# Optimization experiments

Measured on AMD Instinct MI355X. Metric: run time of the kernel, lower is better.

Reference implementation:

```python
import jax, jax.numpy as jnp
import numpy as np


def ste_round(x):
    # straight-through rounding (identity gradient), as used in brevitas fake-quant
    return x + jax.lax.stop_gradient(jnp.round(x) - x)


def quant_weight(w, bits):
    # symmetric per-tensor int quantization: scale = max|w| / (2^(b-1)-1)
    qmax = 2.0 ** (bits - 1) - 1.0
    s = jnp.max(jnp.abs(w)) / qmax
    return jnp.clip(ste_round(w / s), -qmax, qmax) * s


def quant_relu(x, scale, bits):
    # unsigned act quant (QuantReLU): clip to [0, scale], round to 2^b-1 levels
    n = 2.0 ** bits - 1.0
    step = scale / n
    return ste_round(jnp.clip(x, 0.0, scale) / step) * step


def conv2d(x, w, b, pad):
    # NCHW 'same' conv, stride 1
    y = jax.lax.conv_general_dilated(
        x, w, window_strides=(1, 1),
        padding=[(pad, pad), (pad, pad)],
        dimension_numbers=('NCHW', 'OIHW', 'NCHW'))
    return y + b[None, :, None, None]


def setup_inputs() -> dict:
    key = jax.random.key(0)
    ks = jax.random.split(key, 8)
    B, H, W = 8, 512, 512
    x = jax.random.uniform(ks[0], (B, 1, H, W), dtype=jnp.float32)
    # xavier-ish init scales: gain / sqrt(fan_in + fan_out per kernel elem)
    w1 = jax.random.normal(ks[1], (64, 1, 9, 9), dtype=jnp.float32) * 0.12
    b1 = jax.random.normal(ks[2], (64,), dtype=jnp.float32) * 0.01
    w2 = jax.random.normal(ks[3], (32, 64, 5, 5), dtype=jnp.float32) * 0.03
    b2 = jax.random.normal(ks[4], (32,), dtype=jnp.float32) * 0.01
    w3 = jax.random.normal(ks[5], (1, 32, 5, 5), dtype=jnp.float32) * 0.05
    b3 = jax.random.normal(ks[6], (1,), dtype=jnp.float32) * 0.01
    # activation quant scales (learned params in brevitas; fixed here)
    s1 = jnp.ones((1,), dtype=jnp.float32) * 4.0
    s2 = jnp.ones((1,), dtype=jnp.float32) * 4.0
    s3 = jnp.ones((1,), dtype=jnp.float32) * 2.0
    return {"x": x, "w1": w1, "b1": b1, "w2": w2, "b2": b2,
            "w3": w3, "b3": b3, "s1": s1, "s2": s2, "s3": s3}


def reference(x, w1, b1, w2, b2, w3, b3, s1, s2, s3):
    NBK, NBA, NLACT = 8, 8, 8
    # conv1: 1->64, k=9, pad=4, int8 weights; quant-ReLU (nba bits)
    h = conv2d(x, quant_weight(w1, NBK), b1, pad=4)
    h = quant_relu(h, s1[0], NBA)
    # conv2: 64->32, k=5, pad=2
    h = conv2d(h, quant_weight(w2, NBK), b2, pad=2)
    h = quant_relu(h, s2[0], NBA)
    # conv3: 32->1, k=5, pad=2, last-layer weight bits = nlact = 8
    h = conv2d(h, quant_weight(w3, NLACT), b3, pad=2)
    h = quant_relu(h, s3[0], NLACT)
    return h
```

## Files before the change

kernel.cpp:

```cpp
#include <hip/hip_runtime.h>
#include <cmath>

#define HH 512
#define WW 512
#define BB 8
#define WP (WW + 4)
#define HP (HH + 4)

#define PROWS 520
#define PCOLS 528
#define PT ((size_t)BB * PROWS * PCOLS)

typedef int v4i __attribute__((ext_vector_type(4)));
typedef float v4f __attribute__((ext_vector_type(4)));
typedef _Float16 v8h __attribute__((ext_vector_type(8)));

#if defined(__has_builtin)
#if __has_builtin(__builtin_amdgcn_sdot4)
#define DOT4(a, b, c) __builtin_amdgcn_sdot4((a), (b), (c), false)
#endif
#endif
#ifndef DOT4
static __device__ __forceinline__ int dot4_fb(int a, int b, int c) {
  c += ((a << 24) >> 24) * ((b << 24) >> 24);
  c += ((a << 16) >> 24) * ((b << 16) >> 24);
  c += ((a << 8) >> 24) * ((b << 8) >> 24);
  c += (a >> 24) * (b >> 24);
  return c;
}
#define DOT4(a, b, c) dot4_fb((a), (b), (c))
#endif

static constexpr size_t SCALES_OFF = 0;
static constexpr size_t CORRF_OFF  = 64;
static constexpr size_t FS3_OFF    = 512;
static constexpr size_t QW1_OFF    = 1024;
static constexpr size_t W1FRAG_OFF = 24576;
static constexpr size_t W2S_OFF    = 65536;
static constexpr size_t W3P_OFF    = 131072;
static constexpr size_t H1_OFF     = (size_t)1 << 20;
static constexpr size_t H1_SZ      = (size_t)BB * HP * WP * 64;
static constexpr size_t H2_OFF     = H1_OFF + H1_SZ;
static constexpr size_t H2_SZ      = (size_t)BB * HP * WP * 32;
static constexpr size_t WS_NEED    = H2_OFF + H2_SZ;

__global__ void quant_weights_k(const float* __restrict__ w1,
                                const float* __restrict__ w2,
                                const float* __restrict__ w3,
                                float* __restrict__ scales,
                                float* __restrict__ qw1,
                                signed char* __restrict__ w2s,
                                signed char* __restrict__ w3p) {
  const int t = blockIdx.x;
  const float* src = (t == 0) ? w1 : (t == 1) ? w2 : w3;
  const int n = (t == 0) ? 64 * 81 : (t == 1) ? 32 * 64 * 25 : 32 * 25;
  __shared__ float red[256];
  float m = 0.0f;
  for (int i = threadIdx.x; i < n; i += 256) m = fmaxf(m, fabsf(src[i]));
  red[threadIdx.x] = m;
  __syncthreads();
  for (int s = 128; s > 0; s >>= 1) {
    if ((int)threadIdx.x < s) red[threadIdx.x] = fmaxf(red[threadIdx.x], red[threadIdx.x + s]);
    __syncthreads();
  }
  const float scale = red[0] / 127.0f;
  if (threadIdx.x == 0) scales[t] = scale;
  for (int i = threadIdx.x; i < n; i += 256) {
    float q = rintf(src[i] / scale);
    q = fminf(fmaxf(q, -127.0f), 127.0f);
    if (t == 0) {
      qw1[i] = q;
    } else if (t == 1) {
      const int oc = i / 1600;
      const int r = i - oc * 1600;
      const int ic = r / 25, tap = r - ic * 25;
      w2s[(((tap * 4 + (ic >> 4)) * 32) + oc) * 16 + (ic & 15)] = (signed char)(int)q;
    } else {
      const int ic = i / 25, tap = i - ic * 25;
      w3p[tap * 32 + ic] = (signed char)(int)q;
    }
  }
}

__global__ void prep_k(const signed char* __restrict__ w2s,
                       const signed char* __restrict__ w3p,
                       const float* __restrict__ qw1,
                       int* __restrict__ corrf, int* __restrict__ fs3,
                       unsigned short* __restrict__ w1frag) {
  const int tid = threadIdx.x;
  if (tid < 32) {
    int s = 0;
    for (int tap = 0; tap < 25; ++tap)
      for (int kb = 0; kb < 4; ++kb)
        for (int j = 0; j < 16; ++j)
          s += (int)w2s[((tap * 4 + kb) * 32 + tid) * 16 + j];
    corrf[tid] = s;
  } else if (tid == 32) {
    int s = 0;
    for (int i = 0; i < 800; ++i) s += (int)w3p[i];
    fs3[0] = s;
  }
  for (int i = tid; i < 18432; i += 256) {
    const int e = i & 7, lidx = (i >> 3) & 63, nn = (i >> 9) & 3, j = i >> 11;
    const int t = j * 32 + (lidx >> 4) * 8 + e;
    const int term = (t >= 144) ? 1 : 0;
    const int rem = t - term * 144;
    const int ky = rem >> 4, kx = rem & 15;
    const int oc = nn * 16 + (lidx & 15);
    float v = 0.0f;
    if (kx < 9) v = qw1[oc * 81 + ky * 9 + kx];
    if (term) v *= (1.0f / 4096.0f);
    const _Float16 hv = (_Float16)v;
    w1frag[i] = __builtin_bit_cast(unsigned short, hv);
  }
}

__global__ __launch_bounds__(256) void prep_x_k(const float* __restrict__ x,
                                                unsigned short* __restrict__ planes) {
  const size_t i = (size_t)blockIdx.x * 256 + threadIdx.x;
  if (i >= PT) return;
  const int col = (int)(i % PCOLS);
  const size_t t = i / PCOLS;
  const int row = (int)(t % PROWS);
  const int b = (int)(t / PROWS);
  const float* xb = x + (size_t)b * HH * WW;
  const int xr = row - 4;
  float v0 = 0.0f, v1 = 0.0f;
  if (xr >= 0 && xr < HH) {
    const int c0 = col - 4, c1 = col - 3;
    if (c0 >= 0 && c0 < WW) v0 = xb[(size_t)xr * WW + c0];
    if (c1 >= 0 && c1 < WW) v1 = xb[(size_t)xr * WW + c1];
  }
  const _Float16 h0 = (_Float16)v0;
  const _Float16 l0 = (_Float16)((v0 - (float)h0) * 4096.0f);
  const _Float16 h1 = (_Float16)v1;
  const _Float16 l1 = (_Float16)((v1 - (float)h1) * 4096.0f);
  planes[i]          = __builtin_bit_cast(unsigned short, h0);
  planes[PT + i]     = __builtin_bit_cast(unsigned short, l0);
  planes[2 * PT + i] = __builtin_bit_cast(unsigned short, h1);
  planes[3 * PT + i] = __builtin_bit_cast(unsigned short, l1);
}

__global__ void fill_k(unsigned char* __restrict__ h1p, unsigned char* __restrict__ h2p) {
  const int idx = blockIdx.x * 256 + threadIdx.x;
  const uint4 v = make_uint4(0x80808080u, 0x80808080u, 0x80808080u, 0x80808080u);
  if (idx < 66048) {
    const int q = idx & 3; const int u = idx >> 2;
    const int pxi = u % WP; const int rr = u / WP;
    const int bb = rr >> 2, sel = rr & 3;
    const int row = (sel < 2) ? sel : 512 + sel;
    *(uint4*)(h1p + (((size_t)bb * HP + row) * WP + pxi) * 64 + q * 16) = v;
  } else if (idx < 131584) {
    const int e = idx - 66048; const int q = e & 3; int u = e >> 2;
    const int c = u & 3; u >>= 2;
    const int row = 2 + (u & 511); const int bb = u >> 9;
    const int col = (c < 2) ? c : 512 + c;
    *(uint4*)(h1p + (((size_t)bb * HP + row) * WP + col) * 64 + q * 16) = v;
  } else if (idx < 164608) {
    const int e = idx - 131584; const int q = e & 1; const int u = e >> 1;
    const int pxi = u % WP; const int rr = u / WP;
    const int bb = rr >> 2, sel = rr & 3;
    const int row = (sel < 2) ? sel : 512 + sel;
    *(uint4*)(h2p + (((size_t)bb * HP + row) * WP + pxi) * 32 + q * 16) = v;
  } else {
    const int e = idx - 164608; const int q = e & 1; int u = e >> 1;
    const int c = u & 3; u >>= 2;
    const int row = 2 + (u & 511); const int bb = u >> 9;
    const int col = (c < 2) ? c : 512 + c;
    *(uint4*)(h2p + (((size_t)bb * HP + row) * WP + col) * 32 + q * 16) = v;
  }
}

__global__ __launch_bounds__(512) void conv1_k(
    const unsigned short* __restrict__ planes,
    const unsigned short* __restrict__ w1frag,
    const float* __restrict__ b1,
    const float* __restrict__ scales,
    const float* __restrict__ s1,
    unsigned char* __restrict__ h1p) {
  __shared__ alignas(16) unsigned short wf[18432];
  for (int i = threadIdx.x; i < 2304; i += 512)
    ((int4*)wf)[i] = ((const int4*)w1frag)[i];
  __syncthreads();

  const int y = blockIdx.x & (HH - 1);
  const int b = blockIdx.x >> 9;
  const int l = threadIdx.x & 63;
  const int wv = threadIdx.x >> 6;
  const int pxw = wv * 64;
  const int r = l & 15, kb = l >> 4;

  const unsigned short* pb = planes + (size_t)(r & 1) * (2 * PT)
                           + ((size_t)b * PROWS + y) * PCOLS + (pxw + (r & ~1));
  int offs[9];
  #pragma unroll
  for (int j = 0; j < 9; ++j) {
    const int t0 = j * 32 + kb * 8;
    const int term = (t0 >= 144) ? 1 : 0;
    const int rem = t0 - term * 144;
    offs[j] = term * (int)PT + (rem >> 4) * PCOLS + (rem & 8);
  }

  v4f acc[4][4];
  #pragma unroll
  for (int m = 0; m < 4; ++m)
    #pragma unroll
    for (int n = 0; n < 4; ++n) acc[m][n] = (v4f){0.f, 0.f, 0.f, 0.f};

  #pragma unroll
  for (int j = 0; j < 9; ++j) {
    v8h av[4];
    #pragma unroll
    for (int m = 0; m < 4; ++m) {
      const void* ap = __builtin_assume_aligned((const void*)(pb + offs[j] + m * 16), 4);
      uint4 tv;
      __builtin_memcpy(&tv, ap, 16);
      av[m] = __builtin_bit_cast(v8h, tv);
    }
    #pragma unroll
    for (int n = 0; n < 4; ++n) {
      const v8h bv = *(const v8h*)(wf + ((size_t)(j * 4 + n) * 64 + l) * 8);
      #pragma unroll
      for (int m = 0; m < 4; ++m)
        acc[m][n] = __builtin_amdgcn_mfma_f32_16x16x32_f16(av[m], bv, acc[m][n], 0, 0, 0);
    }
  }

  const float ws1 = scales[0];
  const float sc = s1[0], step = sc / 255.0f;
  unsigned char* orow = h1p + (((size_t)b * HP + y + 2) * WP + 2) * 64;
  #pragma unroll
  for (int n = 0; n < 4; ++n) {
    const int oc = n * 16 + r;
    const float bias = b1[oc];
    #pragma unroll
    for (int m = 0; m < 4; ++m) {
      #pragma unroll
      for (int reg = 0; reg < 4; ++reg) {
        const int px = pxw + m * 16 + kb * 4 + reg;
        const float h = acc[m][n][reg] * ws1 + bias;
        const float c = fminf(fmaxf(h, 0.0f), sc);
        int qi = (int)rintf(c / step);
        qi = qi < 0 ? 0 : (qi > 255 ? 255 : qi);
        orow[(size_t)px * 64 + oc] = (unsigned char)(qi ^ 0x80);
      }
    }
  }
}

__global__ __launch_bounds__(256) void conv2_k(
    const unsigned char* __restrict__ h1p,
    const int4* __restrict__ w2s,
    const int* __restrict__ corrf,
    const float* __restrict__ b2,
    const float* __restrict__ scales,
    const float* __restrict__ s1, const float* __restrict__ s2,
    unsigned char* __restrict__ h2p) {
  __shared__ alignas(16) signed char wlds[51200];
  __shared__ int clds[32];
  {
    int4* dst = (int4*)wlds;
    for (int i = threadIdx.x; i < 3200; i += 256) dst[i] = w2s[i];
    if (threadIdx.x < 32) clds[threadIdx.x] = corrf[threadIdx.x];
  }
  __syncthreads();

  const int l = threadIdx.x & 63;
  const int wv = threadIdx.x >> 6;
  const int r = l & 15, kb = l >> 4;
  const int y = blockIdx.y * 4;
  const int b = blockIdx.z;
  const int xw = blockIdx.x * 64 + wv * 16;

  v4i acc[4][2];
  #pragma unroll
  for (int t = 0; t < 4; ++t)
    #pragma unroll
    for (int n = 0; n < 2; ++n) acc[t][n] = (v4i){0, 0, 0, 0};

  const size_t rstride = (size_t)WP * 64;
  const unsigned char* abase = h1p + (((size_t)b * HP + y) * WP + xw + r) * 64 + kb * 16;

  v4i a_cur[8], a_nxt[8];
  #pragma unroll
  for (int j = 0; j < 8; ++j) a_cur[j] = *(const v4i*)(abase + j * rstride);

  #pragma unroll
  for (int kx = 0; kx < 5; ++kx) {
    if (kx < 4) {
      #pragma unroll
      for (int j = 0; j < 8; ++j)
        a_nxt[j] = *(const v4i*)(abase + (kx + 1) * 64 + j * rstride);
    }
    const signed char* bcol = wlds + kx * 2048 + kb * 512 + r * 16;
    #pragma unroll
    for (int ky = 0; ky < 5; ++ky) {
      const v4i bf0 = *(const v4i*)(bcol + ky * 10240);
      const v4i bf1 = *(const v4i*)(bcol + ky * 10240 + 256);
      #pragma unroll
      for (int t = 0; t < 4; ++t) {
        acc[t][0] = __builtin_amdgcn_mfma_i32_16x16x64_i8(a_cur[ky + t], bf0, acc[t][0], 0, 0, 0);
        acc[t][1] = __builtin_amdgcn_mfma_i32_16x16x64_i8(a_cur[ky + t], bf1, acc[t][1], 0, 0, 0);
      }
    }
    if (kx < 4) {
      #pragma unroll
      for (int j = 0; j < 8; ++j) a_cur[j] = a_nxt[j];
    }
  }

  const float step1 = s1[0] / 255.0f;
  const float sc2 = s2[0], step2 = sc2 / 255.0f;
  const float asc = step1 * scales[1];
  #pragma unroll
  for (int n = 0; n < 2; ++n) {
    const int oc = n * 16 + r;
    const float bias = b2[oc];
    const int c128 = clds[oc] * 128;
    #pragma unroll
    for (int t = 0; t < 4; ++t) {
      unsigned char* orow = h2p + (((size_t)b * HP + y + t + 2) * WP + xw + 2) * 32;
      #pragma unroll
      for (int reg = 0; reg < 4; ++reg) {
        const int pxi = kb * 4 + reg;
        const float v = (float)(acc[t][n][reg] + c128) * asc + bias;
        const float c = fminf(fmaxf(v, 0.0f), sc2);
        int qi = (int)rintf(c / step2);
        qi = qi < 0 ? 0 : (qi > 255 ? 255 : qi);
        orow[(size_t)pxi * 32 + oc] = (unsigned char)(qi ^ 0x80);
      }
    }
  }
}

__global__ __launch_bounds__(256) void conv3_k(
    const unsigned char* __restrict__ h2p,
    const signed char* __restrict__ w3p,
    const int* __restrict__ fs3,
    const float* __restrict__ b3,
    const float* __restrict__ scales,
    const float* __restrict__ s2, const float* __restrict__ s3,
    float* __restrict__ out) {
  const int p  = blockIdx.x * 256 + threadIdx.x;
  const int px = p & (WW - 1);
  const int py = (p >> 9) & (HH - 1);
  const int bz = p >> 18;

  int acc = 0;
  const unsigned char* base = h2p + (((size_t)bz * HP + py) * WP + px) * 32;
  #pragma unroll
  for (int ky = 0; ky < 5; ++ky) {
    const unsigned char* rp = base + (size_t)ky * WP * 32;
    #pragma unroll
    for (int kx = 0; kx < 5; ++kx) {
      const int* ap = (const int*)(rp + kx * 32);
      const int* wp = (const int*)(w3p + (ky * 5 + kx) * 32);
      #pragma unroll
      for (int g = 0; g < 8; ++g) acc = DOT4(ap[g], wp[g], acc);
    }
  }

  const int tot = acc + fs3[0] * 128;
  const float step2 = s2[0] / 255.0f;
  const float sc3 = s3[0], step3 = sc3 / 255.0f;
  const float y = (float)tot * (step2 * scales[2]) + b3[0];
  const float c = fminf(fmaxf(y, 0.0f), sc3);
  float q = rintf(c / step3);
  q = fminf(fmaxf(q, 0.0f), 255.0f);
  out[p] = q * step3;
}

extern "C" void kernel_launch(void* const* d_in, const int* in_sizes, int n_in,
                              void* d_out, int out_size, void* d_ws, size_t ws_size,
                              hipStream_t stream) {
  const float* x  = (const float*)d_in[0];
  const float* w1 = (const float*)d_in[1];
  const float* b1 = (const float*)d_in[2];
  const float* w2 = (const float*)d_in[3];
  const float* b2 = (const float*)d_in[4];
  const float* w3 = (const float*)d_in[5];
  const float* b3 = (const float*)d_in[6];
  const float* s1 = (const float*)d_in[7];
  const float* s2 = (const float*)d_in[8];
  const float* s3 = (const float*)d_in[9];

  if (ws_size < WS_NEED) return;

  char* ws = (char*)d_ws;
  float*          scales  = (float*)(ws + SCALES_OFF);
  int*            corrf   = (int*)(ws + CORRF_OFF);
  int*            fs3     = (int*)(ws + FS3_OFF);
  float*          qw1     = (float*)(ws + QW1_OFF);
  unsigned short* w1frag  = (unsigned short*)(ws + W1FRAG_OFF);
  signed char*    w2s     = (signed char*)(ws + W2S_OFF);
  signed char*    w3p     = (signed char*)(ws + W3P_OFF);
  unsigned char*  h1p     = (unsigned char*)(ws + H1_OFF);
  unsigned char*  h2p     = (unsigned char*)(ws + H2_OFF);
  unsigned short* planes  = (unsigned short*)(ws + H2_OFF);

  quant_weights_k<<<3, 256, 0, stream>>>(w1, w2, w3, scales, qw1, w2s, w3p);
  prep_k<<<1, 256, 0, stream>>>(w2s, w3p, qw1, corrf, fs3, w1frag);
  prep_x_k<<<(int)(PT / 256), 256, 0, stream>>>(x, planes);

  conv1_k<<<BB * HH, 512, 0, stream>>>(planes, w1frag, b1, scales, s1, h1p);
  fill_k<<<771, 256, 0, stream>>>(h1p, h2p);

  dim3 g2(8, 128, BB);
  conv2_k<<<g2, 256, 0, stream>>>(h1p, (const int4*)w2s, corrf, b2, scales, s1, s2, h2p);

  const int npix = BB * HH * WW;
  conv3_k<<<npix / 256, 256, 0, stream>>>(h2p, w3p, fs3, b3, scales, s2, s3, (float*)d_out);
}
```

Before: 429.2 us.

## Stage conv1 input tiles in LDS and vectorize conv3 activation loads

conv1 now gives each block a 2-row by 256-pixel tile. The block cooperatively loads all four shifted input planes for that tile into shared memory, and the MFMA A-fragments are then read from LDS instead of global memory, so overlapping global reads are reused across waves. The launch grid changes to match the new tiling. conv3 loads each row's 10 int4 vectors at once and then runs the dot4 products from registers. This adds LDS pressure, which may reduce occupancy in conv1.

```diff
diff --git a/kernel.cpp b/kernel.cpp
--- a/kernel.cpp
+++ b/kernel.cpp
@@ -179,26 +179,46 @@
     const float* __restrict__ s1,
     unsigned char* __restrict__ h1p) {
   __shared__ alignas(16) unsigned short wf[18432];
+  __shared__ alignas(16) unsigned int atile_dw[5440];
+
   for (int i = threadIdx.x; i < 2304; i += 512)
     ((int4*)wf)[i] = ((const int4*)w1frag)[i];
+
+  const int y0  = blockIdx.y * 2;
+  const int xt0 = blockIdx.x * 256;
+  const int b   = blockIdx.z;
+  {
+    const unsigned int* psrc = (const unsigned int*)planes;
+    #pragma unroll
+    for (int it = 0; it < 11; ++it) {
+      const int s = threadIdx.x + it * 512;
+      if (s < 5440) {
+        const int col2 = s % 136;
+        const int rp = s / 136;
+        const int row = rp % 10;
+        const int pt = rp / 10;
+        const size_t gplane = ((size_t)(pt & 1) * 2 + (size_t)(pt >> 1)) * PT;
+        const size_t gsi = gplane + ((size_t)(b * PROWS + y0 + row) * PCOLS + xt0);
+        atile_dw[s] = psrc[gsi / 2 + col2];
+      }
+    }
+  }
   __syncthreads();
 
-  const int y = blockIdx.x & (HH - 1);
-  const int b = blockIdx.x >> 9;
+  const unsigned short* atile = (const unsigned short*)atile_dw;
   const int l = threadIdx.x & 63;
-  const int wv = threadIdx.x >> 6;
-  const int pxw = wv * 64;
+  const int wave = threadIdx.x >> 6;
+  const int wrow = wave & 1, wx = wave >> 1;
   const int r = l & 15, kb = l >> 4;
 
-  const unsigned short* pb = planes + (size_t)(r & 1) * (2 * PT)
-                           + ((size_t)b * PROWS + y) * PCOLS + (pxw + (r & ~1));
+  const int base_l = (r & 1) * 2720 + wrow * 272 + (wx * 64 + (r & ~1));
   int offs[9];
   #pragma unroll
   for (int j = 0; j < 9; ++j) {
     const int t0 = j * 32 + kb * 8;
     const int term = (t0 >= 144) ? 1 : 0;
     const int rem = t0 - term * 144;
-    offs[j] = term * (int)PT + (rem >> 4) * PCOLS + (rem & 8);
+    offs[j] = term * 5440 + (rem >> 4) * 272 + (rem & 8);
   }
 
   v4f acc[4][4];
@@ -209,12 +229,12 @@
 
   #pragma unroll
   for (int j = 0; j < 9; ++j) {
+    const unsigned short* ab = atile + base_l + offs[j];
     v8h av[4];
     #pragma unroll
     for (int m = 0; m < 4; ++m) {
-      const void* ap = __builtin_assume_aligned((const void*)(pb + offs[j] + m * 16), 4);
       uint4 tv;
-      __builtin_memcpy(&tv, ap, 16);
+      __builtin_memcpy(&tv, __builtin_assume_aligned((const void*)(ab + m * 16), 4), 16);
       av[m] = __builtin_bit_cast(v8h, tv);
     }
     #pragma unroll
@@ -228,7 +248,7 @@
 
   const float ws1 = scales[0];
   const float sc = s1[0], step = sc / 255.0f;
-  unsigned char* orow = h1p + (((size_t)b * HP + y + 2) * WP + 2) * 64;
+  unsigned char* orow = h1p + (((size_t)b * HP + y0 + wrow + 2) * WP + 2 + xt0 + wx * 64) * 64;
   #pragma unroll
   for (int n = 0; n < 4; ++n) {
     const int oc = n * 16 + r;
@@ -237,7 +257,7 @@
     for (int m = 0; m < 4; ++m) {
       #pragma unroll
       for (int reg = 0; reg < 4; ++reg) {
-        const int px = pxw + m * 16 + kb * 4 + reg;
+        const int px = m * 16 + kb * 4 + reg;
         const float h = acc[m][n][reg] * ws1 + bias;
         const float c = fminf(fmaxf(h, 0.0f), sc);
         int qi = (int)rintf(c / step);
@@ -346,17 +366,24 @@
   const int py = (p >> 9) & (HH - 1);
   const int bz = p >> 18;
 
+  const int* wq = (const int*)w3p;
+  const unsigned char* base = h2p + (((size_t)bz * HP + py) * WP + px) * 32;
+
   int acc = 0;
-  const unsigned char* base = h2p + (((size_t)bz * HP + py) * WP + px) * 32;
   #pragma unroll
   for (int ky = 0; ky < 5; ++ky) {
-    const unsigned char* rp = base + (size_t)ky * WP * 32;
+    const v4i* rp = (const v4i*)(base + (size_t)ky * WP * 32);
+    v4i c[10];
+    #pragma unroll
+    for (int g = 0; g < 10; ++g) c[g] = rp[g];
+    const int* wrow = wq + ky * 40;
     #pragma unroll
     for (int kx = 0; kx < 5; ++kx) {
-      const int* ap = (const int*)(rp + kx * 32);
-      const int* wp = (const int*)(w3p + (ky * 5 + kx) * 32);
-      #pragma unroll
-      for (int g = 0; g < 8; ++g) acc = DOT4(ap[g], wp[g], acc);
+      #pragma unroll
+      for (int g = 0; g < 8; ++g) {
+        const int idx = kx * 8 + g;
+        acc = DOT4(c[idx >> 2][idx & 3], wrow[idx], acc);
+      }
     }
   }
 
@@ -402,7 +429,8 @@
   prep_k<<<1, 256, 0, stream>>>(w2s, w3p, qw1, corrf, fs3, w1frag);
   prep_x_k<<<(int)(PT / 256), 256, 0, stream>>>(x, planes);
 
-  conv1_k<<<BB * HH, 512, 0, stream>>>(planes, w1frag, b1, scales, s1, h1p);
+  dim3 g1(2, 256, BB);
+  conv1_k<<<g1, 512, 0, stream>>>(planes, w1frag, b1, scales, s1, h1p);
   fill_k<<<771, 256, 0, stream>>>(h1p, h2p);
 
   dim3 g2(8, 128, BB);
```

New measurement: 491.9 us. +14.6%, slower.

## Swap MFMA operands to pack channel bytes into dword stores; vectorize conv3 loads

Applied to the files above, without the earlier changes.

In conv1 and conv2 the MFMA A and B operands are swapped, so each lane's accumulator registers hold four consecutive output channels for one pixel instead of four pixels for one channel. The epilogue then packs the four quantized bytes into a single 32-bit store, replacing scattered single-byte writes. Bias and correction terms are read as vectors to match. conv3 now reads each input row segment with 16-byte vector loads into registers before the dot products. The risk is mistaken index mapping after the transpose, plus some extra register pressure in conv3.

```diff
diff --git a/kernel.cpp b/kernel.cpp
--- a/kernel.cpp
+++ b/kernel.cpp
@@ -203,47 +203,48 @@
 
   v4f acc[4][4];
   #pragma unroll
-  for (int m = 0; m < 4; ++m)
-    #pragma unroll
-    for (int n = 0; n < 4; ++n) acc[m][n] = (v4f){0.f, 0.f, 0.f, 0.f};
+  for (int p = 0; p < 4; ++p)
+    #pragma unroll
+    for (int o = 0; o < 4; ++o) acc[p][o] = (v4f){0.f, 0.f, 0.f, 0.f};
 
   #pragma unroll
   for (int j = 0; j < 9; ++j) {
     v8h av[4];
     #pragma unroll
-    for (int m = 0; m < 4; ++m) {
-      const void* ap = __builtin_assume_aligned((const void*)(pb + offs[j] + m * 16), 4);
+    for (int p = 0; p < 4; ++p) {
+      const void* ap = __builtin_assume_aligned((const void*)(pb + offs[j] + p * 16), 4);
       uint4 tv;
       __builtin_memcpy(&tv, ap, 16);
-      av[m] = __builtin_bit_cast(v8h, tv);
-    }
-    #pragma unroll
-    for (int n = 0; n < 4; ++n) {
-      const v8h bv = *(const v8h*)(wf + ((size_t)(j * 4 + n) * 64 + l) * 8);
-      #pragma unroll
-      for (int m = 0; m < 4; ++m)
-        acc[m][n] = __builtin_amdgcn_mfma_f32_16x16x32_f16(av[m], bv, acc[m][n], 0, 0, 0);
+      av[p] = __builtin_bit_cast(v8h, tv);
+    }
+    #pragma unroll
+    for (int o = 0; o < 4; ++o) {
+      const v8h bw = *(const v8h*)(wf + ((size_t)(j * 4 + o) * 64 + l) * 8);
+      #pragma unroll
+      for (int p = 0; p < 4; ++p)
+        acc[p][o] = __builtin_amdgcn_mfma_f32_16x16x32_f16(bw, av[p], acc[p][o], 0, 0, 0);
     }
   }
 
   const float ws1 = scales[0];
   const float sc = s1[0], step = sc / 255.0f;
-  unsigned char* orow = h1p + (((size_t)b * HP + y + 2) * WP + 2) * 64;
-  #pragma unroll
-  for (int n = 0; n < 4; ++n) {
-    const int oc = n * 16 + r;
-    const float bias = b1[oc];
-    #pragma unroll
-    for (int m = 0; m < 4; ++m) {
+  unsigned int* ob = (unsigned int*)(h1p
+      + (((size_t)b * HP + y + 2) * WP + 2 + pxw + r) * 64 + kb * 4);
+  #pragma unroll
+  for (int o = 0; o < 4; ++o) {
+    const v4f bv = *(const v4f*)(b1 + o * 16 + kb * 4);
+    #pragma unroll
+    for (int p = 0; p < 4; ++p) {
+      unsigned int dw = 0;
       #pragma unroll
       for (int reg = 0; reg < 4; ++reg) {
-        const int px = pxw + m * 16 + kb * 4 + reg;
-        const float h = acc[m][n][reg] * ws1 + bias;
+        const float h = acc[p][o][reg] * ws1 + bv[reg];
         const float c = fminf(fmaxf(h, 0.0f), sc);
         int qi = (int)rintf(c / step);
         qi = qi < 0 ? 0 : (qi > 255 ? 255 : qi);
-        orow[(size_t)px * 64 + oc] = (unsigned char)(qi ^ 0x80);
+        dw |= (unsigned int)(qi ^ 0x80) << (8 * reg);
       }
+      ob[p * 256 + o * 4] = dw;
     }
   }
 }
@@ -257,7 +258,7 @@
     const float* __restrict__ s1, const float* __restrict__ s2,
     unsigned char* __restrict__ h2p) {
   __shared__ alignas(16) signed char wlds[51200];
-  __shared__ int clds[32];
+  __shared__ alignas(16) int clds[32];
   {
     int4* dst = (int4*)wlds;
     for (int i = threadIdx.x; i < 3200; i += 256) dst[i] = w2s[i];
@@ -299,8 +300,8 @@
       const v4i bf1 = *(const v4i*)(bcol + ky * 10240 + 256);
       #pragma unroll
       for (int t = 0; t < 4; ++t) {
-        acc[t][0] = __builtin_amdgcn_mfma_i32_16x16x64_i8(a_cur[ky + t], bf0, acc[t][0], 0, 0, 0);
-        acc[t][1] = __builtin_amdgcn_mfma_i32_16x16x64_i8(a_cur[ky + t], bf1, acc[t][1], 0, 0, 0);
+        acc[t][0] = __builtin_amdgcn_mfma_i32_16x16x64_i8(bf0, a_cur[ky + t], acc[t][0], 0, 0, 0);
+        acc[t][1] = __builtin_amdgcn_mfma_i32_16x16x64_i8(bf1, a_cur[ky + t], acc[t][1], 0, 0, 0);
       }
     }
     if (kx < 4) {
@@ -314,21 +315,22 @@
   const float asc = step1 * scales[1];
   #pragma unroll
   for (int n = 0; n < 2; ++n) {
-    const int oc = n * 16 + r;
-    const float bias = b2[oc];
-    const int c128 = clds[oc] * 128;
+    const v4f bv = *(const v4f*)(b2 + n * 16 + kb * 4);
+    const v4i cv = *(const v4i*)(clds + n * 16 + kb * 4);
     #pragma unroll
     for (int t = 0; t < 4; ++t) {
-      unsigned char* orow = h2p + (((size_t)b * HP + y + t + 2) * WP + xw + 2) * 32;
+      unsigned int* ob = (unsigned int*)(h2p
+          + (((size_t)b * HP + y + t + 2) * WP + xw + 2 + r) * 32 + n * 16 + kb * 4);
+      unsigned int dw = 0;
       #pragma unroll
       for (int reg = 0; reg < 4; ++reg) {
-        const int pxi = kb * 4 + reg;
-        const float v = (float)(acc[t][n][reg] + c128) * asc + bias;
+        const float v = (float)(acc[t][n][reg] + cv[reg] * 128) * asc + bv[reg];
         const float c = fminf(fmaxf(v, 0.0f), sc2);
         int qi = (int)rintf(c / step2);
         qi = qi < 0 ? 0 : (qi > 255 ? 255 : qi);
-        orow[(size_t)pxi * 32 + oc] = (unsigned char)(qi ^ 0x80);
+        dw |= (unsigned int)(qi ^ 0x80) << (8 * reg);
       }
+      *ob = dw;
     }
   }
 }
@@ -346,17 +348,24 @@
   const int py = (p >> 9) & (HH - 1);
   const int bz = p >> 18;
 
+  const int* wq = (const int*)w3p;
+  const unsigned char* base = h2p + (((size_t)bz * HP + py) * WP + px) * 32;
+
   int acc = 0;
-  const unsigned char* base = h2p + (((size_t)bz * HP + py) * WP + px) * 32;
   #pragma unroll
   for (int ky = 0; ky < 5; ++ky) {
-    const unsigned char* rp = base + (size_t)ky * WP * 32;
+    const v4i* rp = (const v4i*)(base + (size_t)ky * WP * 32);
+    v4i c[10];
+    #pragma unroll
+    for (int g = 0; g < 10; ++g) c[g] = rp[g];
+    const int* wrow = wq + ky * 40;
     #pragma unroll
     for (int kx = 0; kx < 5; ++kx) {
-      const int* ap = (const int*)(rp + kx * 32);
-      const int* wp = (const int*)(w3p + (ky * 5 + kx) * 32);
-      #pragma unroll
-      for (int g = 0; g < 8; ++g) acc = DOT4(ap[g], wp[g], acc);
+      #pragma unroll
+      for (int g = 0; g < 8; ++g) {
+        const int idx = kx * 8 + g;
+        acc = DOT4(c[idx >> 2][idx & 3], wrow[idx], acc);
+      }
     }
   }
 
```

Measured after the change: 473.5 us. 10.3% more time.
